# Performance work log

Measured on AMD Instinct MI355X. Metric: run time of the kernel, lower is better.

## Reference

```python
import jax, jax.numpy as jnp
import numpy as np

NUM_PROJS = 7
BLOCK = 256       # HyperAttention block_size
SAMPLE = 256      # HyperAttention sample_size
NUM_HEADS = 16

def _hamming_perm(n):
    a = np.array([0, 1])
    for _ in range(n - 1):
        a = np.concatenate([a, a[::-1] + a.max() + 1])
    return a

_PERM = jnp.asarray(_hamming_perm(NUM_PROJS))           # [128] gray-code-ish bucket reorder
_ENC = (2 ** jnp.arange(NUM_PROJS)).astype(jnp.int32)   # [7]

def _lsh_hash(mat, proj_dir):
    # mat: [B,H,N,d], proj_dir: [d,7] -> bucket ids [B,H,N]
    bits = jnp.einsum('bhnd,dr->bhnr', mat, proj_dir) > 0
    ids = (bits * _ENC).sum(-1)
    return _PERM[ids]

def _attn_lse(q, k, v, scale, bias=None):
    s = jnp.einsum('...qd,...kd->...qk', q, k) * scale
    if bias is not None:
        s = s + bias
    lse = jax.nn.logsumexp(s, axis=-1, keepdims=True)
    o = jnp.einsum('...qk,...kd->...qd', jnp.exp(s - lse), v)
    return o, lse

def _gather(t, idx):
    # gather rows along axis 2: out[b,h,s] = t[b,h,idx[b,h,s]]
    return jnp.take_along_axis(t, idx[..., None], axis=2)

def setup_inputs():
    key = jax.random.key(0)
    ks = jax.random.split(key, 7)
    B, L, D, INNER = 2, 8192, 1024, 1024
    x = jax.random.normal(ks[0], (B, L, D), jnp.float32)
    W_qkv = jax.random.normal(ks[1], (D, 3 * INNER), jnp.float32) / np.sqrt(D)
    b_qkv = jnp.zeros((3 * INNER,), jnp.float32)
    W_proj = jax.random.normal(ks[2], (INNER, D), jnp.float32) / np.sqrt(INNER)
    b_proj = jnp.zeros((D,), jnp.float32)
    proj_dir = jax.random.normal(ks[3], (INNER // NUM_HEADS, NUM_PROJS), jnp.float32)
    sampled_set = jax.random.randint(ks[4], (B, NUM_HEADS, SAMPLE), 0, L)
    return {"x": x, "W_qkv": W_qkv, "b_qkv": b_qkv, "W_proj": W_proj,
            "b_proj": b_proj, "proj_dir": proj_dir, "sampled_set": sampled_set}

def reference(x, W_qkv, b_qkv, W_proj, b_proj, proj_dir, sampled_set):
    B, L, D = x.shape
    qkv = (x @ W_qkv + b_qkv).reshape(B, L, 3, NUM_HEADS, -1).transpose(2, 0, 3, 1, 4)
    q, k, v = qkv[0], qkv[1], qkv[2]                      # [B,H,L,dh]
    dh = q.shape[-1]
    scale = dh ** -0.5
    # 1. sortLSH: stable sort q and k rows by angular-LSH bucket id
    q_idx = jnp.argsort(_lsh_hash(q, proj_dir), axis=2, stable=True)
    k_idx = jnp.argsort(_lsh_hash(k, proj_dir), axis=2, stable=True)
    q_idx_inv = jnp.argsort(q_idx, axis=2, stable=True)   # to restore row order
    qs = _gather(q, q_idx)
    ksort = _gather(k, k_idx)
    vsort = _gather(v, k_idx)
    # block-diagonal exact attention over the sorted order (L % BLOCK == 0 here)
    nb = L // BLOCK
    ab, lb = _attn_lse(qs.reshape(B, NUM_HEADS, nb, BLOCK, dh),
                       ksort.reshape(B, NUM_HEADS, nb, BLOCK, dh),
                       vsort.reshape(B, NUM_HEADS, nb, BLOCK, dh), scale)
    attn_block = ab.reshape(B, NUM_HEADS, L, dh)
    lse_block = lb.reshape(B, NUM_HEADS, L, 1)
    # 2. residual uniformly-sampled attention, masking entries already covered by blocks
    k_sub = _gather(ksort, sampled_set)                   # [B,H,SAMPLE,dh]
    v_sub = _gather(vsort, sampled_set)
    blk_q = jnp.arange(L)[None, None, :, None] // BLOCK   # query block id (query_block_size==BLOCK)
    mask = blk_q == (sampled_set // BLOCK)[:, :, None, :]  # [B,H,L,SAMPLE]
    bias = jnp.where(mask, jnp.finfo(x.dtype).min, 0.0).astype(x.dtype)
    attn_res, lse_res = _attn_lse(qs, k_sub, v_sub, scale, bias)
    lse_res = lse_res + jnp.log(jnp.float32(L) / SAMPLE)  # importance weight n_key/sample_size
    # combine the two attentions via their log-sum-exps
    c = 1.0 / (1.0 + jnp.exp(lse_res - lse_block))
    attn = c * attn_block + (1.0 - c) * attn_res
    out = _gather(attn, q_idx_inv)                        # un-sort rows back to input order
    out = out.transpose(0, 2, 1, 3).reshape(B, L, -1)     # [B,L,inner]
    return out @ W_proj + b_proj
```

## Files before the change

### kernel.cpp

```cpp
#include <hip/hip_runtime.h>
#include <hip/hip_fp16.h>
#include <math.h>


typedef _Float16 f16x8 __attribute__((ext_vector_type(8)));
typedef _Float16 f16x4 __attribute__((ext_vector_type(4)));
typedef __fp16 fp16x2 __attribute__((ext_vector_type(2)));
typedef float f32x4 __attribute__((ext_vector_type(4)));

#define WLIST_CAP 524288
#define TAU 0.06f

__device__ __forceinline__ void gl_lds16(const void* g, void* s) {
    __builtin_amdgcn_global_load_lds(
        (const __attribute__((address_space(1))) unsigned int*)g,
        (__attribute__((address_space(3))) unsigned int*)s, 16, 0, 0);
}

__global__ __launch_bounds__(256) void fold_kernel(
    const float* __restrict__ W, const float* __restrict__ bias,
    const float* __restrict__ proj, double* __restrict__ fold,
    double* __restrict__ bfold, _Float16* __restrict__ foldh,
    float* __restrict__ bfold32)
{
    int idx = blockIdx.x * 256 + threadIdx.x;
    if (idx < 2 * 16 * 7 * 1024) {
        int task = idx / 7168;
        int rem = idx - task * 7168;
        int i = rem / 7;
        int r = rem - i * 7;
        int h = task & 15, w = task >> 4;
        double s = 0.0;
        const float* wp = W + (size_t)i * 3072 + w * 1024 + h * 64;
        for (int d = 0; d < 64; ++d)
            s += (double)wp[d] * (double)proj[d * 7 + r];
        fold[idx] = s;
        foldh[((size_t)task * 7 + r) * 1024 + i] = (_Float16)s;
    }
    if (idx < 32768)
        foldh[229376 + idx] = (_Float16)0.f;
    if (idx < 224) {
        int r = idx % 7;
        int task = idx / 7;
        int h = task & 15, w = task >> 4;
        double s = 0.0;
        for (int d = 0; d < 64; ++d)
            s += (double)bias[w * 1024 + h * 64 + d] * (double)proj[d * 7 + r];
        bfold[idx] = s;
        bfold32[idx] = (float)s;
    }
}

__global__ __launch_bounds__(256) void hashext_kernel(
    const float* __restrict__ scores, const float* __restrict__ bfold32,
    int* __restrict__ hq, int* __restrict__ hk,
    int* __restrict__ wcount, int* __restrict__ wlist)
{
    int tid = blockIdx.x * 256 + threadIdx.x;
    int row = tid >> 5, task = tid & 31;
    const float* sp = scores + (size_t)row * 256 + task * 7;
    int id = 0, fl = 0;
#pragma unroll
    for (int r = 0; r < 7; ++r) {
        float val = sp[r] + bfold32[task * 7 + r];
        if (fabsf(val) < TAU) fl = 1;
        if (val > 0.f) id |= (1 << r);
    }
    int hsh = id ^ (id >> 1);
    int w = task >> 4, h = task & 15;
    int b = row >> 13, l = row & 8191;
    (w ? hk : hq)[((size_t)(b * 16 + h) << 13) + l] = hsh;
    if (fl) {
        int slot = atomicAdd(wcount, 1);
        if (slot < WLIST_CAP) wlist[slot] = task * 16384 + row;
    }
}

__global__ __launch_bounds__(256) void refine_kernel(
    const float* __restrict__ x, const double* __restrict__ fold,
    const double* __restrict__ bfold, const int* __restrict__ wcount,
    const int* __restrict__ wlist, int* __restrict__ hq, int* __restrict__ hk)
{
    int n = *wcount;
    if (n > WLIST_CAP) n = WLIST_CAP;
    int lane = threadIdx.x & 63;
    int wid = (blockIdx.x * 256 + threadIdx.x) >> 6;
    int nw = gridDim.x * 4;
    for (int e = wid; e < n; e += nw) {
        int code = wlist[e];
        int task = code >> 14, grow = code & 16383;
        const double* f = fold + (size_t)task * 7168;
        const float* xp = x + (size_t)grow * 1024;
        double acc[7] = {0, 0, 0, 0, 0, 0, 0};
        for (int i = lane; i < 1024; i += 64) {
            double xv = (double)xp[i];
#pragma unroll
            for (int rr = 0; rr < 7; ++rr)
                acc[rr] = fma(xv, f[(size_t)i * 7 + rr], acc[rr]);
        }
        int id = 0;
#pragma unroll
        for (int rr = 0; rr < 7; ++rr) {
            double a = acc[rr];
#pragma unroll
            for (int off = 32; off > 0; off >>= 1) a += __shfl_xor(a, off, 64);
            if (a + bfold[task * 7 + rr] > 0.0) id |= (1 << rr);
        }
        if (lane == 0) {
            int hsh = id ^ (id >> 1);
            int w = task >> 4, h = task & 15;
            int b = grow >> 13, l = grow & 8191;
            (w ? hk : hq)[((size_t)(b * 16 + h) << 13) + l] = hsh;
        }
    }
}

__global__ __launch_bounds__(256) void sort_kernel(
    const int* __restrict__ hq, const int* __restrict__ hk,
    int* __restrict__ qidx, int* __restrict__ kidx,
    int* __restrict__ qrank, int* __restrict__ krank)
{
    __shared__ unsigned short cnt[128][128];
    __shared__ int tot[128];
    __shared__ int base[128];
    int blk = blockIdx.x;
    int sel = blk >> 5, bh = blk & 31;
    const int* hp = (sel ? hk : hq) + ((size_t)bh << 13);
    int* op = (sel ? kidx : qidx) + ((size_t)bh << 13);
    int* rp = (sel ? krank : qrank) + ((size_t)bh << 13);
    int t = threadIdx.x;
    for (int i = t; i < 128 * 128 / 2; i += 256) ((unsigned int*)cnt)[i] = 0u;
    __syncthreads();
    if (t < 128) {
        const int* p = hp + t * 64;
        for (int j = 0; j < 64; ++j) cnt[t][p[j]]++;
    }
    __syncthreads();
    if (t < 128) {
        int run = 0;
        for (int c = 0; c < 128; ++c) {
            int x2 = cnt[c][t];
            cnt[c][t] = (unsigned short)run;
            run += x2;
        }
        tot[t] = run;
    }
    __syncthreads();
    if (t == 0) {
        int run = 0;
        for (int v = 0; v < 128; ++v) { base[v] = run; run += tot[v]; }
    }
    __syncthreads();
    if (t < 128) {
        const int* p = hp + t * 64;
        for (int j = 0; j < 64; ++j) {
            int v = p[j];
            int c = cnt[t][v];
            cnt[t][v] = (unsigned short)(c + 1);
            int pos = base[v] + c;
            op[pos] = t * 64 + j;
            rp[t * 64 + j] = pos;
        }
    }
}

__global__ __launch_bounds__(256) void castx_kernel(
    const float* __restrict__ x, _Float16* __restrict__ xh)
{
    int i = blockIdx.x * 256 + threadIdx.x;
    float4 f = ((const float4*)x)[i];
    _Float16 h4[4] = {(_Float16)f.x, (_Float16)f.y, (_Float16)f.z, (_Float16)f.w};
    *(short4*)&xh[(size_t)i * 4] = *(short4*)h4;
}

__global__ __launch_bounds__(256) void transpose_kernel(
    const float* __restrict__ W, _Float16* __restrict__ Wt, int K, int N)
{
    __shared__ float tile[32][33];
    int bx = blockIdx.x, by = blockIdx.y;
    int tx = threadIdx.x & 31, ty = threadIdx.x >> 5;
    for (int i = ty; i < 32; i += 8)
        tile[i][tx] = W[(size_t)(by * 32 + i) * N + bx * 32 + tx];
    __syncthreads();
    for (int i = ty; i < 32; i += 8)
        Wt[(size_t)(bx * 32 + i) * K + by * 32 + tx] = (_Float16)tile[tx][i];
}

__global__ __launch_bounds__(256) void gather_samp_kernel(
    const _Float16* __restrict__ ks, const _Float16* __restrict__ vs,
    const int* __restrict__ sampled, _Float16* __restrict__ ksamp,
    _Float16* __restrict__ vsamp)
{
    int bh = blockIdx.x;
    int key = blockIdx.y * 64 + (threadIdx.x >> 2);
    int qtr = (threadIdx.x & 3) * 16;
    size_t hb = (size_t)bh << 13;
    int p = sampled[bh * 256 + key];
    size_t src = (hb + p) * 64 + qtr;
    size_t dst = ((size_t)bh * 256 + key) * 64 + qtr;
    *(f16x8*)(ksamp + dst)     = *(const f16x8*)(ks + src);
    *(f16x8*)(ksamp + dst + 8) = *(const f16x8*)(ks + src + 8);
    *(f16x8*)(vsamp + dst)     = *(const f16x8*)(vs + src);
    *(f16x8*)(vsamp + dst + 8) = *(const f16x8*)(vs + src + 8);
}


template <int MODE>
__global__ __launch_bounds__(256) void mfma_gemm(
    const _Float16* __restrict__ A, const _Float16* __restrict__ Bt,
    const float* __restrict__ bias, float* __restrict__ C, int K, int N)
{
    __shared__ __align__(16) _Float16 As[128 * 64];
    __shared__ __align__(16) _Float16 Bs[128 * 64];
    int t = threadIdx.x;
    int w = t >> 6, l = t & 63;
    int m0 = blockIdx.y * 128, n0 = blockIdx.x * 128;
    int srow = 32 * w + (l >> 3);
    int sslot = ((l & 7) ^ (l >> 3)) * 8;
    const _Float16* ga = A + (size_t)(m0 + srow) * K + sslot;
    const _Float16* gb = Bt + (size_t)(n0 + srow) * K + sslot;
    int wr = w >> 1, wc = w & 1;
    int rl = l & 15, ks = l >> 4;
    f32x4 acc[4][4];
#pragma unroll
    for (int m = 0; m < 4; ++m)
#pragma unroll
        for (int n = 0; n < 4; ++n) acc[m][n] = (f32x4){0.f, 0.f, 0.f, 0.f};
    for (int kk = 0; kk < K; kk += 64) {
        __syncthreads();
#pragma unroll
        for (int i = 0; i < 4; ++i) {
            gl_lds16(ga + (size_t)(8 * i) * K + kk, (char*)As + (32 * w + 8 * i) * 128);
            gl_lds16(gb + (size_t)(8 * i) * K + kk, (char*)Bs + (32 * w + 8 * i) * 128);
        }
        __syncthreads();
        f16x8 af[4][2], bf[4][2];
#pragma unroll
        for (int m = 0; m < 4; ++m) {
            int r = 64 * wr + 16 * m + rl;
            int sw = (r & 7) << 4;
#pragma unroll
            for (int s = 0; s < 2; ++s)
                af[m][s] = *(const f16x8*)((char*)As + r * 128 + (((s * 4 + ks) << 4) ^ sw));
        }
#pragma unroll
        for (int n = 0; n < 4; ++n) {
            int r = 64 * wc + 16 * n + rl;
            int sw = (r & 7) << 4;
#pragma unroll
            for (int s = 0; s < 2; ++s)
                bf[n][s] = *(const f16x8*)((char*)Bs + r * 128 + (((s * 4 + ks) << 4) ^ sw));
        }
#pragma unroll
        for (int m = 0; m < 4; ++m)
#pragma unroll
            for (int n = 0; n < 4; ++n) {
                acc[m][n] = __builtin_amdgcn_mfma_f32_16x16x32_f16(
                    af[m][0], bf[n][0], acc[m][n], 0, 0, 0);
                acc[m][n] = __builtin_amdgcn_mfma_f32_16x16x32_f16(
                    af[m][1], bf[n][1], acc[m][n], 0, 0, 0);
            }
    }
#pragma unroll
    for (int m = 0; m < 4; ++m)
#pragma unroll
        for (int n = 0; n < 4; ++n) {
            int gn = n0 + 64 * wc + 16 * n + rl;
            float bv = (MODE == 2) ? 0.f : bias[gn];
#pragma unroll
            for (int j = 0; j < 4; ++j) {
                int gm = m0 + 64 * wr + 16 * m + 4 * ks + j;
                C[(size_t)gm * N + gn] = acc[m][n][j] + bv;
            }
        }
}

__global__ __launch_bounds__(256) void gemm_qkv_kernel(
    const _Float16* __restrict__ Wt, const _Float16* __restrict__ xh,
    const float* __restrict__ bias, _Float16* __restrict__ Q,
    _Float16* __restrict__ Kb, _Float16* __restrict__ Vb,
    const int* __restrict__ qrank, const int* __restrict__ krank)
{
    const int K = 1024;
    __shared__ __align__(16) _Float16 As[128 * 64];
    __shared__ __align__(16) _Float16 Bs[128 * 64];
    int bid = blockIdx.x;
    int xcd = bid & 7, slot = bid >> 3;
    int y = slot / 3, xl = slot - y * 3;
    int xt = xcd * 3 + xl;
    int m0 = xt * 128;
    int n0 = y * 128;
    int t = threadIdx.x;
    int w = t >> 6, l = t & 63;
    int srow = 32 * w + (l >> 3);
    int sslot = ((l & 7) ^ (l >> 3)) * 8;
    const _Float16* ga = Wt + (size_t)(m0 + srow) * K + sslot;
    const _Float16* gb = xh + (size_t)(n0 + srow) * K + sslot;
    int wr = w >> 1, wc = w & 1;
    int rl = l & 15, ks = l >> 4;
    int fbase = m0 + 64 * wr;
    int s0 = fbase >> 10;
    int h = (fbase >> 6) & 15;
    int b2 = n0 >> 13;
    const int* rk = (s0 == 0) ? qrank : krank;
    _Float16* dst = (s0 == 0) ? Q : (s0 == 1 ? Kb : Vb);
    size_t bhb = ((size_t)(b2 * 16 + h) << 13);
    int tl = (n0 & 8191) + 64 * wc;
    int pos[4];
#pragma unroll
    for (int n = 0; n < 4; ++n)
        pos[n] = rk[bhb + tl + 16 * n + rl];
    float4 bias4[4];
#pragma unroll
    for (int m = 0; m < 4; ++m)
        bias4[m] = *(const float4*)&bias[fbase + 16 * m + 4 * ks];
    f32x4 acc[4][4];
#pragma unroll
    for (int m = 0; m < 4; ++m)
#pragma unroll
        for (int n = 0; n < 4; ++n) acc[m][n] = (f32x4){0.f, 0.f, 0.f, 0.f};
    for (int kk = 0; kk < K; kk += 64) {
        __syncthreads();
#pragma unroll
        for (int i = 0; i < 4; ++i) {
            gl_lds16(ga + (size_t)(8 * i) * K + kk, (char*)As + (32 * w + 8 * i) * 128);
            gl_lds16(gb + (size_t)(8 * i) * K + kk, (char*)Bs + (32 * w + 8 * i) * 128);
        }
        __syncthreads();
        f16x8 af[4][2], bf[4][2];
#pragma unroll
        for (int m = 0; m < 4; ++m) {
            int r = 64 * wr + 16 * m + rl;
            int sw = (r & 7) << 4;
#pragma unroll
            for (int s = 0; s < 2; ++s)
                af[m][s] = *(const f16x8*)((char*)As + r * 128 + (((s * 4 + ks) << 4) ^ sw));
        }
#pragma unroll
        for (int n = 0; n < 4; ++n) {
            int r = 64 * wc + 16 * n + rl;
            int sw = (r & 7) << 4;
#pragma unroll
            for (int s = 0; s < 2; ++s)
                bf[n][s] = *(const f16x8*)((char*)Bs + r * 128 + (((s * 4 + ks) << 4) ^ sw));
        }
#pragma unroll
        for (int m = 0; m < 4; ++m)
#pragma unroll
            for (int n = 0; n < 4; ++n) {
                acc[m][n] = __builtin_amdgcn_mfma_f32_16x16x32_f16(
                    af[m][0], bf[n][0], acc[m][n], 0, 0, 0);
                acc[m][n] = __builtin_amdgcn_mfma_f32_16x16x32_f16(
                    af[m][1], bf[n][1], acc[m][n], 0, 0, 0);
            }
    }
#pragma unroll
    for (int m = 0; m < 4; ++m)
#pragma unroll
        for (int n = 0; n < 4; ++n) {
            f16x4 st;
            st[0] = (_Float16)(acc[m][n][0] + bias4[m].x);
            st[1] = (_Float16)(acc[m][n][1] + bias4[m].y);
            st[2] = (_Float16)(acc[m][n][2] + bias4[m].z);
            st[3] = (_Float16)(acc[m][n][3] + bias4[m].w);
            *(f16x4*)(dst + (bhb + pos[n]) * 64 + 16 * m + 4 * ks) = st;
        }
}

__global__ __launch_bounds__(256) void attn_mfma_kernel(
    const _Float16* __restrict__ qs_, const _Float16* __restrict__ ks_,
    const _Float16* __restrict__ vs_, const _Float16* __restrict__ ksamp,
    const _Float16* __restrict__ vsamp, const int* __restrict__ qidx,
    const int* __restrict__ sampled, _Float16* __restrict__ pre)
{
    __shared__ __align__(16) _Float16 Vt[2][64 * 68];
    int bid = blockIdx.x;
    int nb = (bid & 7) * 256 + (bid >> 3);
    int bh = nb >> 6, qb = (nb >> 1) & 31, half = nb & 1;
    int bb = bh >> 4, hh = bh & 15;
    size_t hb = (size_t)bh << 13;
    size_t bhs = (size_t)bh * 256;
    int t = threadIdx.x;
    int w = t >> 6, l = t & 63;
    int g = l >> 4, c16 = l & 15;
    int kg = t & 15, dg = t >> 4;
    int qw0 = qb * 256 + half * 128 + w * 32;
    const _Float16 qs = (_Float16)0.125f;

    int orig[2];
    f16x8 qf[2][2];
#pragma unroll
    for (int n = 0; n < 2; ++n) {
        int row = qw0 + 16 * n + c16;
        orig[n] = qidx[hb + row];
        const _Float16* qp = qs_ + (hb + row) * 64 + g * 8;
        qf[n][0] = *(const f16x8*)(qp);
        qf[n][1] = *(const f16x8*)(qp + 32);
#pragma unroll
        for (int j = 0; j < 8; ++j) { qf[n][0][j] *= qs; qf[n][1][j] *= qs; }
    }
    f32x4 o[4][2];
    float mr[2], lr[2];
#pragma unroll
    for (int n = 0; n < 2; ++n) {
        mr[n] = -1e30f; lr[n] = 0.f;
#pragma unroll
        for (int d2 = 0; d2 < 4; ++d2) o[d2][n] = (f32x4){0.f, 0.f, 0.f, 0.f};
    }
    const float LOG32 = 3.4657359027997265f;

    {
        const _Float16* vb = vs_ + (hb + qb * 256) * 64;
        f16x4 vr[4];
#pragma unroll
        for (int j2 = 0; j2 < 4; ++j2)
            vr[j2] = *(const f16x4*)(vb + (4 * kg + j2) * 64 + 4 * dg);
#pragma unroll
        for (int i = 0; i < 4; ++i) {
            f16x4 o4 = {vr[0][i], vr[1][i], vr[2][i], vr[3][i]};
            *(f16x4*)&Vt[0][(4 * dg + i) * 68 + 4 * kg] = o4;
        }
    }

    for (int c = 0; c < 8; ++c) {
        int cur = c & 1, nxt = cur ^ 1;
        bool samp = c >= 4;
        __syncthreads();
        const _Float16* kb = samp ? ksamp + (bhs + (size_t)(c - 4) * 64) * 64
                                  : ks_ + (hb + qb * 256 + (size_t)c * 64) * 64;
        f16x8 kf[4][2];
#pragma unroll
        for (int m = 0; m < 4; ++m) {
            const _Float16* kp = kb + (16 * m + c16) * 64 + g * 8;
            kf[m][0] = *(const f16x8*)(kp);
            kf[m][1] = *(const f16x8*)(kp + 32);
        }
        int4 spv[4];
        if (samp) {
#pragma unroll
            for (int m = 0; m < 4; ++m)
                spv[m] = *(const int4*)(sampled + bhs + (c - 4) * 64 + 16 * m + 4 * g);
        }
        f32x4 sacc[4][2];
#pragma unroll
        for (int m = 0; m < 4; ++m)
#pragma unroll
            for (int n = 0; n < 2; ++n) sacc[m][n] = (f32x4){0.f, 0.f, 0.f, 0.f};
#pragma unroll
        for (int m = 0; m < 4; ++m) {
#pragma unroll
            for (int n = 0; n < 2; ++n)
                sacc[m][n] = __builtin_amdgcn_mfma_f32_16x16x32_f16(
                    kf[m][0], qf[n][0], sacc[m][n], 0, 0, 0);
#pragma unroll
            for (int n = 0; n < 2; ++n)
                sacc[m][n] = __builtin_amdgcn_mfma_f32_16x16x32_f16(
                    kf[m][1], qf[n][1], sacc[m][n], 0, 0, 0);
        }
        f16x4 vrn[4];
        if (c < 7) {
            const _Float16* vb = (c + 1 >= 4)
                ? vsamp + (bhs + (size_t)(c - 3) * 64) * 64
                : vs_ + (hb + qb * 256 + (size_t)(c + 1) * 64) * 64;
#pragma unroll
            for (int j2 = 0; j2 < 4; ++j2)
                vrn[j2] = *(const f16x4*)(vb + (4 * kg + j2) * 64 + 4 * dg);
        }
        f16x4 av[4][4];
#pragma unroll
        for (int m = 0; m < 4; ++m)
#pragma unroll
            for (int d2 = 0; d2 < 4; ++d2)
                av[m][d2] = *(const f16x4*)&Vt[cur][(16 * d2 + c16) * 68 + 16 * m + 4 * g];
        bool msk[4][4];
#pragma unroll
        for (int m = 0; m < 4; ++m) {
            msk[m][0] = samp && ((spv[m].x >> 8) == qb);
            msk[m][1] = samp && ((spv[m].y >> 8) == qb);
            msk[m][2] = samp && ((spv[m].z >> 8) == qb);
            msk[m][3] = samp && ((spv[m].w >> 8) == qb);
        }
        float badd = samp ? LOG32 : 0.f;
#pragma unroll
        for (int n = 0; n < 2; ++n) {
            float sv[16];
#pragma unroll
            for (int m = 0; m < 4; ++m)
#pragma unroll
                for (int r = 0; r < 4; ++r)
                    sv[4 * m + r] = msk[m][r] ? -1e30f : sacc[m][n][r] + badd;
            float a0 = fmaxf(fmaxf(sv[0], sv[1]), sv[2]);
            float a1 = fmaxf(fmaxf(sv[3], sv[4]), sv[5]);
            float a2 = fmaxf(fmaxf(sv[6], sv[7]), sv[8]);
            float a3 = fmaxf(fmaxf(sv[9], sv[10]), sv[11]);
            float a4 = fmaxf(fmaxf(sv[12], sv[13]), sv[14]);
            float cm = fmaxf(fmaxf(fmaxf(a0, a1), a2), fmaxf(fmaxf(a3, a4), sv[15]));
            cm = fmaxf(cm, __shfl_xor(cm, 16, 64));
            cm = fmaxf(cm, __shfl_xor(cm, 32, 64));
            if (__any(cm > mr[n])) {
                float nm = fmaxf(mr[n], cm);
                float fq = __expf(mr[n] - nm);
                mr[n] = nm;
                lr[n] *= fq;
#pragma unroll
                for (int d2 = 0; d2 < 4; ++d2) {
                    o[d2][n][0] *= fq; o[d2][n][1] *= fq;
                    o[d2][n][2] *= fq; o[d2][n][3] *= fq;
                }
            }
            float pv16[16];
#pragma unroll
            for (int r = 0; r < 16; ++r) pv16[r] = __expf(sv[r] - mr[n]);
            float s0 = (pv16[0] + pv16[1]) + (pv16[2] + pv16[3]);
            float s1 = (pv16[4] + pv16[5]) + (pv16[6] + pv16[7]);
            float s2 = (pv16[8] + pv16[9]) + (pv16[10] + pv16[11]);
            float s3 = (pv16[12] + pv16[13]) + (pv16[14] + pv16[15]);
            float ps = (s0 + s1) + (s2 + s3);
            ps += __shfl_xor(ps, 16, 64);
            ps += __shfl_xor(ps, 32, 64);
            lr[n] += ps;
            f16x4 pb[4];
#pragma unroll
            for (int m = 0; m < 4; ++m) {
                fp16x2 c0 = __builtin_amdgcn_cvt_pkrtz(pv16[4 * m + 0], pv16[4 * m + 1]);
                fp16x2 c1 = __builtin_amdgcn_cvt_pkrtz(pv16[4 * m + 2], pv16[4 * m + 3]);
                pb[m][0] = (_Float16)c0[0]; pb[m][1] = (_Float16)c0[1];
                pb[m][2] = (_Float16)c1[0]; pb[m][3] = (_Float16)c1[1];
            }
#pragma unroll
            for (int d2 = 0; d2 < 4; ++d2)
#pragma unroll
                for (int m = 0; m < 4; ++m)
                    o[d2][n] = __builtin_amdgcn_mfma_f32_16x16x16f16(
                        av[m][d2], pb[m], o[d2][n], 0, 0, 0);
        }
        if (c < 7) {
#pragma unroll
            for (int i = 0; i < 4; ++i) {
                f16x4 o4 = {vrn[0][i], vrn[1][i], vrn[2][i], vrn[3][i]};
                *(f16x4*)&Vt[nxt][(4 * dg + i) * 68 + 4 * kg] = o4;
            }
        }
    }
#pragma unroll
    for (int n = 0; n < 2; ++n) {
        float invl = 1.f / lr[n];
        _Float16* pp = pre + ((size_t)(bb * 8192 + orig[n])) * 1024 + hh * 64;
#pragma unroll
        for (int d2 = 0; d2 < 4; ++d2) {
            f16x4 st;
            st[0] = (_Float16)(o[d2][n][0] * invl);
            st[1] = (_Float16)(o[d2][n][1] * invl);
            st[2] = (_Float16)(o[d2][n][2] * invl);
            st[3] = (_Float16)(o[d2][n][3] * invl);
            *(f16x4*)(pp + 16 * d2 + 4 * g) = st;
        }
    }
}

extern "C" void kernel_launch(void* const* d_in, const int* in_sizes, int n_in,
                              void* d_out, int out_size, void* d_ws, size_t ws_size,
                              hipStream_t stream)
{
    (void)in_sizes; (void)n_in; (void)out_size; (void)ws_size;
    const float* x     = (const float*)d_in[0];
    const float* Wqkv  = (const float*)d_in[1];
    const float* bqkv  = (const float*)d_in[2];
    const float* Wproj = (const float*)d_in[3];
    const float* bproj = (const float*)d_in[4];
    const float* proj  = (const float*)d_in[5];
    const int*   samp  = (const int*)d_in[6];
    float* out = (float*)d_out;

    char* ws = (char*)d_ws;
    size_t off = 0;
    auto take = [&](size_t bytes) {
        char* p = ws + off;
        off = (off + bytes + 255) & ~(size_t)255;
        return p;
    };
    _Float16* xh  = (_Float16*)take(33554432);
    _Float16* q   = (_Float16*)take(33554432);
    _Float16* k   = (_Float16*)take(33554432);
    _Float16* v   = (_Float16*)take(33554432);
    float* scores = (float*)take(16777216);
    _Float16* Wtq = (_Float16*)take(6291456);
    _Float16* Wtp = (_Float16*)take(2097152);
    _Float16* foldh = (_Float16*)take(524288);
    _Float16* ksamp = (_Float16*)take(1048576);
    _Float16* vsamp = (_Float16*)take(1048576);
    double* fold   = (double*)take(1835008);
    double* bfold  = (double*)take(1792);
    float* bfold32 = (float*)take(896);
    int* wcount = (int*)take(256);
    int* wlist  = (int*)take(WLIST_CAP * 4);
    int* hq    = (int*)take(1048576);
    int* hk    = (int*)take(1048576);
    int* qidx  = (int*)take(1048576);
    int* kidx  = (int*)take(1048576);
    int* qrank = (int*)take(1048576);
    int* krank = (int*)take(1048576);
    _Float16* pre = xh;

    (void)hipMemsetAsync(wcount, 0, 4, stream);
    castx_kernel<<<dim3(16384), dim3(256), 0, stream>>>(x, xh);
    fold_kernel<<<dim3(896), dim3(256), 0, stream>>>(
        Wqkv, bqkv, proj, fold, bfold, foldh, bfold32);
    mfma_gemm<2><<<dim3(2, 128), dim3(256), 0, stream>>>(
        xh, foldh, nullptr, scores, 1024, 256);
    hashext_kernel<<<dim3(2048), dim3(256), 0, stream>>>(
        scores, bfold32, hq, hk, wcount, wlist);
    refine_kernel<<<dim3(2048), dim3(256), 0, stream>>>(
        x, fold, bfold, wcount, wlist, hq, hk);
    sort_kernel<<<dim3(64), dim3(256), 0, stream>>>(
        hq, hk, qidx, kidx, qrank, krank);
    transpose_kernel<<<dim3(96, 32), dim3(256), 0, stream>>>(Wqkv, Wtq, 1024, 3072);
    transpose_kernel<<<dim3(32, 32), dim3(256), 0, stream>>>(Wproj, Wtp, 1024, 1024);
    gemm_qkv_kernel<<<dim3(3072), dim3(256), 0, stream>>>(
        Wtq, xh, bqkv, q, k, v, qrank, krank);
    gather_samp_kernel<<<dim3(32, 4), dim3(256), 0, stream>>>(
        k, v, samp, ksamp, vsamp);
    attn_mfma_kernel<<<dim3(2048), dim3(256), 0, stream>>>(
        q, k, v, ksamp, vsamp, qidx, samp, pre);
    mfma_gemm<0><<<dim3(8, 128), dim3(256), 0, stream>>>(
        pre, Wtp, bproj, out, 1024, 1024);
}
```

Before: 561.2 us.

## Rewrite QKV GEMM with 256x256 tiles and double-buffered async LDS pipeline

The QKV projection GEMM now uses 512-thread blocks, each computing a 256x256 output tile. It double-buffers LDS through 128KB of dynamic shared memory and issues global-to-LDS loads for the next k-tiles interleaved with MFMA groups, with raised wave priority around the MFMAs. The aim is to hide global load latency behind compute and raise arithmetic intensity per LDS byte. The cost is high register pressure from 32 accumulators per wave, fewer blocks (768), and one block per CU because of the large LDS footprint.

```diff
diff --git a/kernel.cpp b/kernel.cpp
--- a/kernel.cpp
+++ b/kernel.cpp
@@ -204,7 +204,6 @@
     *(f16x8*)(vsamp + dst + 8) = *(const f16x8*)(vs + src + 8);
 }
 
-
 template <int MODE>
 __global__ __launch_bounds__(256) void mfma_gemm(
     const _Float16* __restrict__ A, const _Float16* __restrict__ Bt,
@@ -275,87 +274,153 @@
         }
 }
 
-__global__ __launch_bounds__(256) void gemm_qkv_kernel(
+__global__ __launch_bounds__(512) void gemm_qkv_kernel(
     const _Float16* __restrict__ Wt, const _Float16* __restrict__ xh,
     const float* __restrict__ bias, _Float16* __restrict__ Q,
     _Float16* __restrict__ Kb, _Float16* __restrict__ Vb,
     const int* __restrict__ qrank, const int* __restrict__ krank)
 {
+    extern __shared__ __align__(16) char smem[];
     const int K = 1024;
-    __shared__ __align__(16) _Float16 As[128 * 64];
-    __shared__ __align__(16) _Float16 Bs[128 * 64];
     int bid = blockIdx.x;
     int xcd = bid & 7, slot = bid >> 3;
-    int y = slot / 3, xl = slot - y * 3;
-    int xt = xcd * 3 + xl;
-    int m0 = xt * 128;
-    int n0 = y * 128;
+    int ty = slot / 12, tx = slot - ty * 12;
+    int m0 = tx * 256;
+    int n0 = (xcd * 8 + ty) * 256;
     int t = threadIdx.x;
     int w = t >> 6, l = t & 63;
-    int srow = 32 * w + (l >> 3);
-    int sslot = ((l & 7) ^ (l >> 3)) * 8;
-    const _Float16* ga = Wt + (size_t)(m0 + srow) * K + sslot;
-    const _Float16* gb = xh + (size_t)(n0 + srow) * K + sslot;
-    int wr = w >> 1, wc = w & 1;
+    int wr = w >> 2, wc = w & 3;
     int rl = l & 15, ks = l >> 4;
-    int fbase = m0 + 64 * wr;
+    int srow = t >> 3;
+    int sslot = (t & 7) ^ ((t >> 3) & 7);
+    const _Float16* gA = Wt + (size_t)m0 * K + sslot * 8;
+    const _Float16* gB = xh + (size_t)n0 * K + sslot * 8;
+    char* dstT = smem + t * 16;
+
+    auto STAGE = [&](int buf, int op, int half, int kt) {
+        const _Float16* src = op ? gB : gA;
+        char* d = dstT + buf * 65536 + op * 32768 + half * 16384;
+        size_t ro = (size_t)(half * 128 + srow) * K + kt * 64;
+        gl_lds16(src + ro, d);
+        gl_lds16(src + ro + (size_t)64 * K, d + 8192);
+    };
+
+    int fbase = m0 + 128 * wr;
     int s0 = fbase >> 10;
-    int h = (fbase >> 6) & 15;
+    int h0 = (fbase >> 6) & 15;
     int b2 = n0 >> 13;
     const int* rk = (s0 == 0) ? qrank : krank;
-    _Float16* dst = (s0 == 0) ? Q : (s0 == 1 ? Kb : Vb);
-    size_t bhb = ((size_t)(b2 * 16 + h) << 13);
+    _Float16* dq = (s0 == 0) ? Q : (s0 == 1 ? Kb : Vb);
     int tl = (n0 & 8191) + 64 * wc;
-    int pos[4];
-#pragma unroll
-    for (int n = 0; n < 4; ++n)
-        pos[n] = rk[bhb + tl + 16 * n + rl];
-    float4 bias4[4];
-#pragma unroll
-    for (int m = 0; m < 4; ++m)
+    int pos[2][4];
+#pragma unroll
+    for (int hf = 0; hf < 2; ++hf)
+#pragma unroll
+        for (int n = 0; n < 4; ++n)
+            pos[hf][n] = rk[((size_t)(b2 * 16 + h0 + hf) << 13) + tl + 16 * n + rl];
+    float4 bias4[8];
+#pragma unroll
+    for (int m = 0; m < 8; ++m)
         bias4[m] = *(const float4*)&bias[fbase + 16 * m + 4 * ks];
-    f32x4 acc[4][4];
-#pragma unroll
-    for (int m = 0; m < 4; ++m)
+
+    f32x4 acc[8][4];
+#pragma unroll
+    for (int m = 0; m < 8; ++m)
 #pragma unroll
         for (int n = 0; n < 4; ++n) acc[m][n] = (f32x4){0.f, 0.f, 0.f, 0.f};
-    for (int kk = 0; kk < K; kk += 64) {
-        __syncthreads();
-#pragma unroll
-        for (int i = 0; i < 4; ++i) {
-            gl_lds16(ga + (size_t)(8 * i) * K + kk, (char*)As + (32 * w + 8 * i) * 128);
-            gl_lds16(gb + (size_t)(8 * i) * K + kk, (char*)Bs + (32 * w + 8 * i) * 128);
-        }
-        __syncthreads();
-        f16x8 af[4][2], bf[4][2];
-#pragma unroll
-        for (int m = 0; m < 4; ++m) {
-            int r = 64 * wr + 16 * m + rl;
-            int sw = (r & 7) << 4;
-#pragma unroll
-            for (int s = 0; s < 2; ++s)
-                af[m][s] = *(const f16x8*)((char*)As + r * 128 + (((s * 4 + ks) << 4) ^ sw));
-        }
+
+    STAGE(0, 0, 0, 0); STAGE(0, 0, 1, 0); STAGE(0, 1, 0, 0); STAGE(0, 1, 1, 0);
+    STAGE(1, 1, 0, 1); STAGE(1, 1, 1, 1);
+
+    for (int tt = 0; tt < 16; ++tt) {
+        int buf = tt & 1, obuf = buf ^ 1;
+        if (tt < 15) asm volatile("s_waitcnt vmcnt(4)" ::: "memory");
+        else         asm volatile("s_waitcnt vmcnt(0)" ::: "memory");
+        __builtin_amdgcn_sched_barrier(0);
+        __builtin_amdgcn_s_barrier();
+        __builtin_amdgcn_sched_barrier(0);
+        const char* Ab = smem + buf * 65536;
+        const char* Bb = Ab + 32768;
+        f16x8 bf[4][2], af01[2][2];
 #pragma unroll
         for (int n = 0; n < 4; ++n) {
             int r = 64 * wc + 16 * n + rl;
             int sw = (r & 7) << 4;
-#pragma unroll
-            for (int s = 0; s < 2; ++s)
-                bf[n][s] = *(const f16x8*)((char*)Bs + r * 128 + (((s * 4 + ks) << 4) ^ sw));
-        }
-#pragma unroll
-        for (int m = 0; m < 4; ++m)
+            bf[n][0] = *(const f16x8*)(Bb + r * 128 + ((ks << 4) ^ sw));
+            bf[n][1] = *(const f16x8*)(Bb + r * 128 + (((4 + ks) << 4) ^ sw));
+        }
+#pragma unroll
+        for (int m = 0; m < 2; ++m) {
+            int r = 128 * wr + 16 * m + rl;
+            int sw = (r & 7) << 4;
+            af01[m][0] = *(const f16x8*)(Ab + r * 128 + ((ks << 4) ^ sw));
+            af01[m][1] = *(const f16x8*)(Ab + r * 128 + (((4 + ks) << 4) ^ sw));
+        }
+        if (tt + 1 < 16) STAGE(obuf, 0, 0, tt + 1);
+        __builtin_amdgcn_s_setprio(1);
+#pragma unroll
+        for (int m = 0; m < 2; ++m)
 #pragma unroll
             for (int n = 0; n < 4; ++n) {
                 acc[m][n] = __builtin_amdgcn_mfma_f32_16x16x32_f16(
-                    af[m][0], bf[n][0], acc[m][n], 0, 0, 0);
+                    af01[m][0], bf[n][0], acc[m][n], 0, 0, 0);
                 acc[m][n] = __builtin_amdgcn_mfma_f32_16x16x32_f16(
-                    af[m][1], bf[n][1], acc[m][n], 0, 0, 0);
-            }
-    }
-#pragma unroll
-    for (int m = 0; m < 4; ++m)
+                    af01[m][1], bf[n][1], acc[m][n], 0, 0, 0);
+            }
+        __builtin_amdgcn_s_setprio(0);
+        f16x8 af27[6][2];
+#pragma unroll
+        for (int m = 0; m < 6; ++m) {
+            int r = 128 * wr + 16 * (m + 2) + rl;
+            int sw = (r & 7) << 4;
+            af27[m][0] = *(const f16x8*)(Ab + r * 128 + ((ks << 4) ^ sw));
+            af27[m][1] = *(const f16x8*)(Ab + r * 128 + (((4 + ks) << 4) ^ sw));
+        }
+        if (tt + 1 < 16) STAGE(obuf, 0, 1, tt + 1);
+        __builtin_amdgcn_s_setprio(1);
+#pragma unroll
+        for (int m = 0; m < 2; ++m)
+#pragma unroll
+            for (int n = 0; n < 4; ++n) {
+                acc[m + 2][n] = __builtin_amdgcn_mfma_f32_16x16x32_f16(
+                    af27[m][0], bf[n][0], acc[m + 2][n], 0, 0, 0);
+                acc[m + 2][n] = __builtin_amdgcn_mfma_f32_16x16x32_f16(
+                    af27[m][1], bf[n][1], acc[m + 2][n], 0, 0, 0);
+            }
+        __builtin_amdgcn_s_setprio(0);
+        asm volatile("" ::: "memory");
+        __builtin_amdgcn_s_barrier();
+        __builtin_amdgcn_sched_barrier(0);
+        if (tt + 2 < 16) STAGE(buf, 1, 0, tt + 2);
+        __builtin_amdgcn_s_setprio(1);
+#pragma unroll
+        for (int m = 2; m < 4; ++m)
+#pragma unroll
+            for (int n = 0; n < 4; ++n) {
+                acc[m + 2][n] = __builtin_amdgcn_mfma_f32_16x16x32_f16(
+                    af27[m][0], bf[n][0], acc[m + 2][n], 0, 0, 0);
+                acc[m + 2][n] = __builtin_amdgcn_mfma_f32_16x16x32_f16(
+                    af27[m][1], bf[n][1], acc[m + 2][n], 0, 0, 0);
+            }
+        __builtin_amdgcn_s_setprio(0);
+        if (tt + 2 < 16) STAGE(buf, 1, 1, tt + 2);
+        __builtin_amdgcn_s_setprio(1);
+#pragma unroll
+        for (int m = 4; m < 6; ++m)
+#pragma unroll
+            for (int n = 0; n < 4; ++n) {
+                acc[m + 2][n] = __builtin_amdgcn_mfma_f32_16x16x32_f16(
+                    af27[m][0], bf[n][0], acc[m + 2][n], 0, 0, 0);
+                acc[m + 2][n] = __builtin_amdgcn_mfma_f32_16x16x32_f16(
+                    af27[m][1], bf[n][1], acc[m + 2][n], 0, 0, 0);
+            }
+        __builtin_amdgcn_s_setprio(0);
+    }
+#pragma unroll
+    for (int m = 0; m < 8; ++m) {
+        int hf = m >> 2;
+        size_t bhb = ((size_t)(b2 * 16 + h0 + hf) << 13);
+        int d = 16 * (m & 3) + 4 * ks;
 #pragma unroll
         for (int n = 0; n < 4; ++n) {
             f16x4 st;
@@ -363,8 +428,9 @@
             st[1] = (_Float16)(acc[m][n][1] + bias4[m].y);
             st[2] = (_Float16)(acc[m][n][2] + bias4[m].z);
             st[3] = (_Float16)(acc[m][n][3] + bias4[m].w);
-            *(f16x4*)(dst + (bhb + pos[n]) * 64 + 16 * m + 4 * ks) = st;
-        }
+            *(f16x4*)(dq + (bhb + pos[hf][n]) * 64 + d) = st;
+        }
+    }
 }
 
 __global__ __launch_bounds__(256) void attn_mfma_kernel(
@@ -602,6 +668,8 @@
     int* krank = (int*)take(1048576);
     _Float16* pre = xh;
 
+    (void)hipFuncSetAttribute((const void*)gemm_qkv_kernel,
+                              hipFuncAttributeMaxDynamicSharedMemorySize, 131072);
     (void)hipMemsetAsync(wcount, 0, 4, stream);
     castx_kernel<<<dim3(16384), dim3(256), 0, stream>>>(x, xh);
     fold_kernel<<<dim3(896), dim3(256), 0, stream>>>(
@@ -616,7 +684,7 @@
         hq, hk, qidx, kidx, qrank, krank);
     transpose_kernel<<<dim3(96, 32), dim3(256), 0, stream>>>(Wqkv, Wtq, 1024, 3072);
     transpose_kernel<<<dim3(32, 32), dim3(256), 0, stream>>>(Wproj, Wtp, 1024, 1024);
-    gemm_qkv_kernel<<<dim3(3072), dim3(256), 0, stream>>>(
+    gemm_qkv_kernel<<<dim3(768), dim3(512), 131072, stream>>>(
         Wtq, xh, bqkv, q, k, v, qrank, krank);
     gather_samp_kernel<<<dim3(32, 4), dim3(256), 0, stream>>>(
         k, v, samp, ksamp, vsamp);
```

New measurement: 550.6 us. Within noise of the previous version (-1.9%).
